# Performance work log

Measured on AMD Instinct MI355X. Metric: run time of the kernel, lower is better.

The kernel has to match this reference:

```python
import jax, jax.numpy as jnp
import numpy as np

BS, T, E, H, CU = 8, 1024, 512, 8, 6
HD = E // H
W_SCALE = 0.05  # keep pre-softmax logits in a sane range


def setup_inputs() -> dict:
    key = jax.random.key(0)
    ks = jax.random.split(key, 9)
    return {
        "x": jax.random.normal(ks[0], (BS, T, E), jnp.float32),
        "u": jax.random.normal(ks[1], (BS, CU, T, T), jnp.float32),
        "umask": jnp.zeros((BS, T, T, 1), jnp.bool_),
        "wq": jax.random.normal(ks[2], (E, E), jnp.float32) * W_SCALE,
        "wk": jax.random.normal(ks[3], (E, E), jnp.float32) * W_SCALE,
        "wv": jax.random.normal(ks[4], (E, E), jnp.float32) * W_SCALE,
        "wo": jax.random.normal(ks[5], (E, E), jnp.float32) * W_SCALE,
        "bo": jnp.zeros((E,), jnp.float32),
        "wu": jax.random.normal(ks[6], (H, CU), jnp.float32) * W_SCALE,
        "bu": jnp.zeros((H,), jnp.float32),
    }


def reference(x, u, umask, wq, wk, wv, wo, bo, wu, bu):
    bs, t, e = x.shape
    h, hd = H, HD
    scaling = hd ** (-0.5)

    # linear projections (torch Linear: y = x @ W^T), split heads -> [b, h, t, hd]
    def proj(w):
        return jnp.einsum('bte,fe->btf', x, w).reshape(bs, t, h, hd).transpose(0, 2, 1, 3)

    Q, K, V = proj(wq), proj(wk), proj(wv)

    # NOTE: faithful to source, which DIVIDES by head_dim**-0.5
    scores = jnp.einsum('bhqd,bhkd->bhqk', Q, K) / scaling

    # 1x1 conv bias projection: [b, cu, t, t] -> [b, h, t, t]
    ubias = jnp.einsum('bcij,hc->bhij', u, wu) + bu[None, :, None, None]
    # umask: [b, t, t, 1] -> swap dims 1 and 3 -> [b, 1, t, t]
    mask_t = jnp.transpose(umask, (0, 3, 2, 1))
    ubias = jnp.where(mask_t, -jnp.inf, ubias)
    scores = scores + ubias

    attn = jax.nn.softmax(scores, axis=-1)
    # dropout p=0.0 -> identity
    ctx = jnp.einsum('bhqk,bhkd->bqhd', attn, V).reshape(bs, t, e)
    out = jnp.einsum('bte,fe->btf', ctx, wo) + bo
    return (out, attn)
```

## Files before the change

### kernel.cpp

```cpp
#include <hip/hip_runtime.h>
#include <cmath>

#define BSZ 8
#define TT  1024
#define EE  512
#define HH  8
#define CUc 6
#define HDD 64

typedef __bf16 bf16;
typedef __attribute__((ext_vector_type(4))) float f32x4;
typedef __attribute__((ext_vector_type(8))) float f32x8;
typedef __attribute__((ext_vector_type(4))) bf16  bf16x4;
typedef __attribute__((ext_vector_type(8))) bf16  bf16x8;

static __device__ __forceinline__ f32x4 mfma16(bf16x8 a, bf16x8 b, f32x4 c) {
    return __builtin_amdgcn_mfma_f32_16x16x32_bf16(a, b, c, 0, 0, 0);
}
static __device__ __forceinline__ void glds16(const bf16* g, bf16* l) {
    __builtin_amdgcn_global_load_lds((const __attribute__((address_space(1))) void*)g,
                                     (__attribute__((address_space(3))) void*)l, 16, 0, 0);
}

__global__ __launch_bounds__(256) void k_split_all(
    const float* __restrict__ wq, const float* __restrict__ wk,
    const float* __restrict__ wv, const float* __restrict__ wo,
    bf16* __restrict__ wqh, bf16* __restrict__ wql,
    bf16* __restrict__ wkh, bf16* __restrict__ wkl,
    bf16* __restrict__ wvh, bf16* __restrict__ woh)
{
    const float* src; bf16* hi; bf16* lo;
    switch (blockIdx.y) {
        case 0: src = wq; hi = wqh; lo = wql;     break;
        case 1: src = wk; hi = wkh; lo = wkl;     break;
        case 2: src = wv; hi = wvh; lo = nullptr; break;
        default: src = wo; hi = woh; lo = nullptr; break;
    }
    const int i = (blockIdx.x * 256 + threadIdx.x) * 8;
    f32x8 v = *(const f32x8*)(src + i);
    bf16x8 h8, l8;
#pragma unroll
    for (int k = 0; k < 8; ++k) {
        bf16 h = (bf16)v[k];
        h8[k] = h;
        l8[k] = (bf16)(v[k] - (float)h);
    }
    *(bf16x8*)(hi + i) = h8;
    if (lo) *(bf16x8*)(lo + i) = l8;
}

__global__ __launch_bounds__(256) void k_proj2(
    const float* __restrict__ x,
    const bf16* __restrict__ wqh, const bf16* __restrict__ wql,
    const bf16* __restrict__ wkh, const bf16* __restrict__ wkl,
    const bf16* __restrict__ wvh,
    bf16* __restrict__ Qh, bf16* __restrict__ Ql,
    bf16* __restrict__ Kh, bf16* __restrict__ Kl,
    bf16* __restrict__ Vt)
{
    const int rb = blockIdx.x;
    const int cb = blockIdx.y;
    const int wid = threadIdx.x >> 6;
    const int l   = threadIdx.x & 63;
    const int lg = l >> 4, lr = l & 15;
    const int row = rb * 64 + wid * 16 + lr;

    f32x4 aq[4], ak[4], av[4];
#pragma unroll
    for (int c = 0; c < 4; ++c) {
        aq[c] = f32x4{0.f,0.f,0.f,0.f}; ak[c] = f32x4{0.f,0.f,0.f,0.f}; av[c] = f32x4{0.f,0.f,0.f,0.f};
    }

    for (int ks = 0; ks < 16; ++ks) {
        const int e0 = ks * 32 + lg * 8;
        f32x8 xv = *(const f32x8*)(x + (size_t)row * EE + e0);
        bf16x8 xh, xl;
#pragma unroll
        for (int i = 0; i < 8; ++i) {
            bf16 h = (bf16)xv[i];
            xh[i] = h;
            xl[i] = (bf16)(xv[i] - (float)h);
        }
#pragma unroll
        for (int c = 0; c < 4; ++c) {
            const int f = cb * 64 + c * 16 + lr;
            const size_t wo = (size_t)f * EE + e0;
            bf16x8 qh = *(const bf16x8*)(wqh + wo);
            bf16x8 ql = *(const bf16x8*)(wql + wo);
            bf16x8 kh = *(const bf16x8*)(wkh + wo);
            bf16x8 kl = *(const bf16x8*)(wkl + wo);
            bf16x8 vh = *(const bf16x8*)(wvh + wo);
            aq[c] = mfma16(xh, qh, aq[c]); aq[c] = mfma16(xh, ql, aq[c]); aq[c] = mfma16(xl, qh, aq[c]);
            ak[c] = mfma16(xh, kh, ak[c]); ak[c] = mfma16(xh, kl, ak[c]); ak[c] = mfma16(xl, kh, ak[c]);
            av[c] = mfma16(xh, vh, av[c]);
        }
    }

#pragma unroll
    for (int c = 0; c < 4; ++c)
#pragma unroll
        for (int r = 0; r < 4; ++r) {
            const int orow = rb * 64 + wid * 16 + lg * 4 + r;
            const int b = orow >> 10, t = orow & 1023;
            const int f = cb * 64 + c * 16 + lr;
            const int h = f >> 6, d = f & 63;
            const size_t idx = ((size_t)(b * HH + h) * TT + t) * HDD + d;
            float vq = aq[c][r];
            bf16 qhi = (bf16)vq; Qh[idx] = qhi; Ql[idx] = (bf16)(vq - (float)qhi);
            float vk = ak[c][r];
            bf16 khi = (bf16)vk; Kh[idx] = khi; Kl[idx] = (bf16)(vk - (float)khi);
            Vt[(((size_t)(b * HH + h) * HDD + d) * TT) + t] = (bf16)av[c][r];
        }
}

__global__ __launch_bounds__(256) void k_ubias2(
    const float* __restrict__ u, const unsigned char* __restrict__ umask,
    const float* __restrict__ wu, const float* __restrict__ bu,
    float* __restrict__ A)
{
    __shared__ __align__(16) unsigned char msk[64][64];
    const int b  = blockIdx.z;
    const int i0 = blockIdx.y * 64;
    const int j0 = blockIdx.x * 64;
    const int t  = threadIdx.x;

    {
        const int jj  = t >> 2;
        const int seg = (t & 3) * 16;
        *(uint4*)(&msk[jj][seg]) =
            *(const uint4*)(umask + ((size_t)b * TT + (j0 + jj)) * TT + i0 + seg);
    }
    float wuv[HH][CUc], buv[HH];
#pragma unroll
    for (int h = 0; h < HH; ++h) {
        buv[h] = bu[h];
#pragma unroll
        for (int c = 0; c < CUc; ++c) wuv[h][c] = wu[h * CUc + c];
    }
    __syncthreads();

    const int j = j0 + (t & 63);
    for (int ii = (t >> 6); ii < 64; ii += 4) {
        const int i = i0 + ii;
        float uv[CUc];
#pragma unroll
        for (int c = 0; c < CUc; ++c)
            uv[c] = u[(((size_t)b * CUc + c) * TT + i) * TT + j];
        const bool mk = msk[t & 63][ii] != 0;
#pragma unroll
        for (int h = 0; h < HH; ++h) {
            float v = buv[h];
#pragma unroll
            for (int c = 0; c < CUc; ++c) v += uv[c] * wuv[h][c];
            if (mk) v = -INFINITY;
            bf16* ub = (bf16*)(A + ((size_t)(b * HH + h) * TT + (i & ~15)) * TT);
            ub[(i & 15) * TT + j] = (bf16)v;
        }
    }
}

__global__ __launch_bounds__(512, 1) void kf10(
    const bf16* __restrict__ Qh, const bf16* __restrict__ Ql,
    const bf16* __restrict__ Kh, const bf16* __restrict__ Kl,
    const bf16* __restrict__ Vt,
    float* __restrict__ A, bf16* __restrict__ ctx)
{
    const int g  = blockIdx.x;
    const int b  = g & 7;
    const int hh = g >> 6;
    const int ib = (g >> 3) & 7;
    const int bh = b * HH + hh;
    const int i0 = ib * 128;
    const int w  = threadIdx.x >> 6;
    const int l  = threadIdx.x & 63;
    const int lg = l >> 4, lr = l & 15;
    const int i16c = ib * 8 + w;
    const int iw   = i0 + w * 16;

    __shared__ __align__(16) bf16 KHL[2][8192];
    __shared__ __align__(16) bf16 KLL[2][8192];
    __shared__ __align__(16) bf16 VL [2][8192];
    __shared__ __align__(16) bf16 P  [8][2048];
    __shared__ float mh[8][16][12];

    const bf16* KhG = Kh + (size_t)bh * TT * HDD;
    const bf16* KlG = Kl + (size_t)bh * TT * HDD;
    const bf16* VtG = Vt + (size_t)bh * HDD * TT;
    bf16* Aw = (bf16*)(A + ((size_t)bh * TT + i16c * 16) * TT);

    const bf16* qph = Qh + ((size_t)bh * TT + iw) * HDD;
    const bf16* qpl = Ql + ((size_t)bh * TT + iw) * HDD;
    bf16x8 qh0 = *(const bf16x8*)(qph + lr * HDD + lg * 8);
    bf16x8 qh1 = *(const bf16x8*)(qph + lr * HDD + 32 + lg * 8);
    bf16x8 ql0 = *(const bf16x8*)(qpl + lr * HDD + lg * 8);
    bf16x8 ql1 = *(const bf16x8*)(qpl + lr * HDD + 32 + lg * 8);

    auto stage = [&](int buf, int t) {
        const int j0 = t * 128;
#pragma unroll
        for (int k = 0; k < 6; ++k) {
            const int gu = w * 6 + k;
            if (gu < 16) {
                const int u = gu;
                const int jr = u * 8 + (l >> 3), s = l & 7;
                glds16(KhG + (size_t)(j0 + jr) * HDD + ((s ^ (jr & 7)) * 8),
                       &KHL[buf][u * 512]);
            } else if (gu < 32) {
                const int u = gu - 16;
                const int jr = u * 8 + (l >> 3), s = l & 7;
                glds16(KlG + (size_t)(j0 + jr) * HDD + ((s ^ (jr & 7)) * 8),
                       &KLL[buf][u * 512]);
            } else {
                const int u = gu - 32;
                const int d = u * 4 + (l >> 4), s = l & 15;
                const int q = (s & 8) | ((s ^ (d & 7)) & 7);
                glds16(VtG + (size_t)d * TT + j0 + q * 8,
                       &VL[buf][u * 512]);
            }
        }
    };

    float m_run[4], s_run[4];
    f32x4 cacc[4];
#pragma unroll
    for (int r = 0; r < 4; ++r) { m_run[r] = -INFINITY; s_run[r] = 0.f; }
#pragma unroll
    for (int dt = 0; dt < 4; ++dt) cacc[dt] = f32x4{0.f,0.f,0.f,0.f};

    stage(0, 0);
    __syncthreads();

    for (int t = 0; t < 8; ++t) {
        const int buf = t & 1;

        bf16x8 ubr[4];
#pragma unroll
        for (int q = 0; q < 4; ++q) {
            const int r = q * 4 + (l >> 4), s = l & 15;
            ubr[q] = *(const bf16x8*)(Aw + (size_t)r * TT + t * 128 + s * 8);
        }
        if (t < 7) stage(buf ^ 1, t + 1);

        f32x4 s8[8];
#pragma unroll
        for (int jt2 = 0; jt2 < 8; ++jt2) {
            const int jr = jt2 * 16 + lr;
            const int x7 = jr & 7;
            bf16x8 kh0 = *(const bf16x8*)&KHL[buf][jr * 64 + ((lg       ^ x7) * 8)];
            bf16x8 kh1 = *(const bf16x8*)&KHL[buf][jr * 64 + (((lg + 4) ^ x7) * 8)];
            bf16x8 kl0 = *(const bf16x8*)&KLL[buf][jr * 64 + ((lg       ^ x7) * 8)];
            bf16x8 kl1 = *(const bf16x8*)&KLL[buf][jr * 64 + (((lg + 4) ^ x7) * 8)];
            f32x4 acc = f32x4{0.f,0.f,0.f,0.f};
            acc = mfma16(qh0, kh0, acc); acc = mfma16(qh1, kh1, acc);
            acc = mfma16(qh0, kl0, acc); acc = mfma16(qh1, kl1, acc);
            acc = mfma16(ql0, kh0, acc); acc = mfma16(ql1, kh1, acc);
            s8[jt2] = acc;
        }

#pragma unroll
        for (int q = 0; q < 4; ++q) {
            const int r = q * 4 + (l >> 4), s = l & 15;
            const int slot = (s & 8) | ((s ^ (r & 7)) & 7);
            *(bf16x8*)&P[w][r * 128 + slot * 8] = ubr[q];
        }
#pragma unroll
        for (int jt2 = 0; jt2 < 8; ++jt2)
#pragma unroll
            for (int r = 0; r < 4; ++r) {
                const int row = lg * 4 + r, col = jt2 * 16 + lr;
                const int sg = col >> 3;
                const int slot = (sg & 8) | ((sg ^ (row & 7)) & 7);
                s8[jt2][r] = s8[jt2][r] * 8.0f + (float)P[w][row * 128 + slot * 8 + (col & 7)];
            }

        float tm[4];
#pragma unroll
        for (int r = 0; r < 4; ++r) {
            float mm = s8[0][r];
#pragma unroll
            for (int jt2 = 1; jt2 < 8; ++jt2) mm = fmaxf(mm, s8[jt2][r]);
            tm[r] = mm;
        }
#pragma unroll
        for (int off = 1; off < 16; off <<= 1)
#pragma unroll
            for (int r = 0; r < 4; ++r) tm[r] = fmaxf(tm[r], __shfl_xor(tm[r], off));
        float mnew[4], mexp[4], e[4];
#pragma unroll
        for (int r = 0; r < 4; ++r) {
            mnew[r] = fmaxf(m_run[r], tm[r]);
            mexp[r] = (mnew[r] == -INFINITY) ? 0.f : mnew[r];
            e[r]    = (m_run[r] == -INFINITY) ? 0.f : __expf(m_run[r] - mexp[r]);
            m_run[r] = mnew[r];
        }
#pragma unroll
        for (int dt = 0; dt < 4; ++dt)
#pragma unroll
            for (int r = 0; r < 4; ++r) cacc[dt][r] *= e[r];

        float psum[4] = {0.f, 0.f, 0.f, 0.f};
#pragma unroll
        for (int jt2 = 0; jt2 < 8; ++jt2)
#pragma unroll
            for (int r = 0; r < 4; ++r) {
                const float p = __expf(s8[jt2][r] - mexp[r]);
                psum[r] += p;
                const int row = lg * 4 + r, col = jt2 * 16 + lr;
                const int sg = col >> 3;
                const int slot = (sg & 8) | ((sg ^ (row & 7)) & 7);
                P[w][row * 128 + slot * 8 + (col & 7)] = (bf16)p;
            }
#pragma unroll
        for (int off = 1; off < 16; off <<= 1)
#pragma unroll
            for (int r = 0; r < 4; ++r) psum[r] += __shfl_xor(psum[r], off);
#pragma unroll
        for (int r = 0; r < 4; ++r) s_run[r] = s_run[r] * e[r] + psum[r];
        if (lr == 0)
#pragma unroll
            for (int r = 0; r < 4; ++r) mh[w][lg * 4 + r][t] = mnew[r];

#pragma unroll
        for (int q = 0; q < 4; ++q) {
            const int r = q * 4 + (l >> 4), s = l & 15;
            const int slot = (s & 8) | ((s ^ (r & 7)) & 7);
            bf16x8 pv = *(const bf16x8*)&P[w][r * 128 + slot * 8];
            *(bf16x8*)(Aw + (size_t)r * 2048 + 1024 + t * 128 + s * 8) = pv;
        }

#pragma unroll
        for (int ks = 0; ks < 4; ++ks) {
            const int sg = ks * 4 + lg;
            const int ps = (sg & 8) | ((sg ^ (lr & 7)) & 7);
            bf16x8 a = *(const bf16x8*)&P[w][lr * 128 + ps * 8];
#pragma unroll
            for (int dt = 0; dt < 4; ++dt) {
                const int d = dt * 16 + lr;
                const int vs = (sg & 8) | ((sg ^ (d & 7)) & 7);
                bf16x8 bv = *(const bf16x8*)&VL[buf][d * 128 + vs * 8];
                cacc[dt] = mfma16(a, bv, cacc[dt]);
            }
        }
        __syncthreads();
    }

    if (lr == 0)
#pragma unroll
        for (int r = 0; r < 4; ++r) mh[w][lg * 4 + r][8] = s_run[r];

    float invS[4], mfin[4];
#pragma unroll
    for (int q = 0; q < 4; ++q) {
        const int r = q * 4 + (l >> 4);
        mfin[q] = mh[w][r][7];
        invS[q] = 1.0f / mh[w][r][8];
    }
    float* Af = A + ((size_t)bh * TT + i16c * 16) * TT;
#pragma unroll
    for (int t = 0; t < 8; ++t) {
        bf16x8 pv[4];
        float fac[4];
#pragma unroll
        for (int q = 0; q < 4; ++q) {
            const int r = q * 4 + (l >> 4), s = l & 15;
            pv[q] = *(const bf16x8*)(Aw + (size_t)r * 2048 + 1024 + t * 128 + s * 8);
            fac[q] = __expf(mh[w][r][t] - mfin[q]) * invS[q];
        }
        asm volatile("s_waitcnt vmcnt(0)" ::: "memory");
#pragma unroll
        for (int q = 0; q < 4; ++q) {
            const int r = q * 4 + (l >> 4), s = l & 15;
            f32x4 o0, o1;
#pragma unroll
            for (int ee = 0; ee < 4; ++ee) {
                o0[ee] = (float)pv[q][ee]     * fac[q];
                o1[ee] = (float)pv[q][4 + ee] * fac[q];
            }
            *(f32x4*)(Af + (size_t)r * TT + t * 128 + s * 8)     = o0;
            *(f32x4*)(Af + (size_t)r * TT + t * 128 + s * 8 + 4) = o1;
        }
    }

#pragma unroll
    for (int r = 0; r < 4; ++r) {
        const float is = 1.0f / s_run[r];
        const int row = iw + lg * 4 + r;
#pragma unroll
        for (int dt = 0; dt < 4; ++dt)
            ctx[((size_t)b * TT + row) * EE + hh * HDD + dt * 16 + lr] = (bf16)(cacc[dt][r] * is);
    }
}

__global__ __launch_bounds__(256) void k_out2(
    const bf16* __restrict__ ctx, const bf16* __restrict__ woh,
    const float* __restrict__ bo, float* __restrict__ out)
{
    const int rb = blockIdx.x;
    const int cb = blockIdx.y;
    const int wid = threadIdx.x >> 6;
    const int l = threadIdx.x & 63;
    const int lg = l >> 4, lr = l & 15;
    const int row = rb * 64 + wid * 16 + lr;

    f32x4 acc[4];
#pragma unroll
    for (int c = 0; c < 4; ++c) acc[c] = f32x4{0.f,0.f,0.f,0.f};

    for (int ks = 0; ks < 16; ++ks) {
        const int e0 = ks * 32 + lg * 8;
        bf16x8 af = *(const bf16x8*)(ctx + (size_t)row * EE + e0);
#pragma unroll
        for (int c = 0; c < 4; ++c) {
            const int f = cb * 64 + c * 16 + lr;
            bf16x8 wf = *(const bf16x8*)(woh + (size_t)f * EE + e0);
            acc[c] = mfma16(af, wf, acc[c]);
        }
    }
#pragma unroll
    for (int c = 0; c < 4; ++c) {
        const int f = cb * 64 + c * 16 + lr;
        const float bov = bo[f];
#pragma unroll
        for (int r = 0; r < 4; ++r) {
            const int orow = rb * 64 + wid * 16 + lg * 4 + r;
            out[(size_t)orow * EE + f] = acc[c][r] + bov;
        }
    }
}

extern "C" void kernel_launch(void* const* d_in, const int* in_sizes, int n_in,
                              void* d_out, int out_size, void* d_ws, size_t ws_size,
                              hipStream_t stream)
{
    (void)in_sizes; (void)n_in; (void)out_size; (void)ws_size;
    const float* x  = (const float*)d_in[0];
    const float* u  = (const float*)d_in[1];
    const unsigned char* umask = (const unsigned char*)d_in[2];
    const float* wq = (const float*)d_in[3];
    const float* wk = (const float*)d_in[4];
    const float* wv = (const float*)d_in[5];
    const float* wo = (const float*)d_in[6];
    const float* bo = (const float*)d_in[7];
    const float* wu = (const float*)d_in[8];
    const float* bu = (const float*)d_in[9];

    float* out = (float*)d_out;
    float* A   = out + (size_t)BSZ * TT * EE;

    const size_t qs  = (size_t)BSZ * HH * TT * HDD;
    const size_t wsz = (size_t)EE * EE;
    bf16* Qh  = (bf16*)d_ws;
    bf16* Ql  = Qh + qs;
    bf16* Kh  = Ql + qs;
    bf16* Kl  = Kh + qs;
    bf16* Vt  = Kl + qs;
    bf16* ctx = Vt + qs;
    bf16* wqh = ctx + qs;
    bf16* wql = wqh + wsz;
    bf16* wkh = wql + wsz;
    bf16* wkl = wkh + wsz;
    bf16* wvh = wkl + wsz;
    bf16* woh = wvh + wsz;

    k_split_all<<<dim3(128, 4), 256, 0, stream>>>(wq, wk, wv, wo,
                                                  wqh, wql, wkh, wkl, wvh, woh);
    k_ubias2<<<dim3(16, 16, 8), 256, 0, stream>>>(u, umask, wu, bu, A);
    k_proj2 <<<dim3(128, 8), 256, 0, stream>>>(x, wqh, wql, wkh, wkl, wvh, Qh, Ql, Kh, Kl, Vt);
    kf10    <<<512, 512, 0, stream>>>(Qh, Ql, Kh, Kl, Vt, A, ctx);
    k_out2  <<<dim3(128, 8), 256, 0, stream>>>(ctx, woh, bo, out);
}
```

Baseline: 441.1 us.

## Halve attention key tile to 64 to cut LDS and allow more blocks per CU

The fused attention kernel now processes keys in 64-wide tiles over 16 iterations instead of 128-wide tiles over 8. This halves the shared-memory buffers for K, V and P, and the launch bound asks for 4 blocks per CU instead of 1, aiming at higher occupancy and better latency hiding. The cost is twice as many barriers and online-softmax rescale steps, plus a changed swizzle and a simpler final normalization pass. The projection and bias kernel launches are also swapped in order.

New measurement: 530.4 us. +20.2%, slower.

```diff
diff --git a/kernel.cpp b/kernel.cpp
--- a/kernel.cpp
+++ b/kernel.cpp
@@ -159,7 +159,7 @@
     }
 }
 
-__global__ __launch_bounds__(512, 1) void kf10(
+__global__ __launch_bounds__(512, 4) void kf10b(
     const bf16* __restrict__ Qh, const bf16* __restrict__ Ql,
     const bf16* __restrict__ Kh, const bf16* __restrict__ Kl,
     const bf16* __restrict__ Vt,
@@ -177,11 +177,11 @@
     const int i16c = ib * 8 + w;
     const int iw   = i0 + w * 16;
 
-    __shared__ __align__(16) bf16 KHL[2][8192];
-    __shared__ __align__(16) bf16 KLL[2][8192];
-    __shared__ __align__(16) bf16 VL [2][8192];
-    __shared__ __align__(16) bf16 P  [8][2048];
-    __shared__ float mh[8][16][12];
+    __shared__ __align__(16) bf16 KHL[2][4096];
+    __shared__ __align__(16) bf16 KLL[2][4096];
+    __shared__ __align__(16) bf16 VL [2][4096];
+    __shared__ __align__(16) bf16 P  [8][1024];
+    __shared__ float mh[8][16][18];
 
     const bf16* KhG = Kh + (size_t)bh * TT * HDD;
     const bf16* KlG = Kl + (size_t)bh * TT * HDD;
@@ -196,25 +196,23 @@
     bf16x8 ql1 = *(const bf16x8*)(qpl + lr * HDD + 32 + lg * 8);
 
     auto stage = [&](int buf, int t) {
-        const int j0 = t * 128;
-#pragma unroll
-        for (int k = 0; k < 6; ++k) {
-            const int gu = w * 6 + k;
-            if (gu < 16) {
-                const int u = gu;
-                const int jr = u * 8 + (l >> 3), s = l & 7;
+        const int j0 = t * 64;
+#pragma unroll
+        for (int k = 0; k < 3; ++k) {
+            const int gu = w * 3 + k;
+            if (gu < 8) {
+                const int jr = gu * 8 + (l >> 3), s = l & 7;
                 glds16(KhG + (size_t)(j0 + jr) * HDD + ((s ^ (jr & 7)) * 8),
-                       &KHL[buf][u * 512]);
-            } else if (gu < 32) {
-                const int u = gu - 16;
+                       &KHL[buf][gu * 512]);
+            } else if (gu < 16) {
+                const int u = gu - 8;
                 const int jr = u * 8 + (l >> 3), s = l & 7;
                 glds16(KlG + (size_t)(j0 + jr) * HDD + ((s ^ (jr & 7)) * 8),
                        &KLL[buf][u * 512]);
             } else {
-                const int u = gu - 32;
-                const int d = u * 4 + (l >> 4), s = l & 15;
-                const int q = (s & 8) | ((s ^ (d & 7)) & 7);
-                glds16(VtG + (size_t)d * TT + j0 + q * 8,
+                const int u = gu - 16;
+                const int d = u * 8 + (l >> 3), s = l & 7;
+                glds16(VtG + (size_t)d * TT + j0 + ((s ^ (d & 7)) * 8),
                        &VL[buf][u * 512]);
             }
         }
@@ -230,20 +228,20 @@
     stage(0, 0);
     __syncthreads();
 
-    for (int t = 0; t < 8; ++t) {
+    for (int t = 0; t < 16; ++t) {
         const int buf = t & 1;
 
-        bf16x8 ubr[4];
-#pragma unroll
-        for (int q = 0; q < 4; ++q) {
-            const int r = q * 4 + (l >> 4), s = l & 15;
-            ubr[q] = *(const bf16x8*)(Aw + (size_t)r * TT + t * 128 + s * 8);
-        }
-        if (t < 7) stage(buf ^ 1, t + 1);
-
-        f32x4 s8[8];
-#pragma unroll
-        for (int jt2 = 0; jt2 < 8; ++jt2) {
+        bf16x8 ubr[2];
+#pragma unroll
+        for (int q = 0; q < 2; ++q) {
+            const int r = q * 8 + (l >> 3), s = l & 7;
+            ubr[q] = *(const bf16x8*)(Aw + (size_t)r * TT + t * 64 + s * 8);
+        }
+        if (t < 15) stage(buf ^ 1, t + 1);
+
+        f32x4 s8[4];
+#pragma unroll
+        for (int jt2 = 0; jt2 < 4; ++jt2) {
             const int jr = jt2 * 16 + lr;
             const int x7 = jr & 7;
             bf16x8 kh0 = *(const bf16x8*)&KHL[buf][jr * 64 + ((lg       ^ x7) * 8)];
@@ -258,19 +256,18 @@
         }
 
 #pragma unroll
-        for (int q = 0; q < 4; ++q) {
-            const int r = q * 4 + (l >> 4), s = l & 15;
-            const int slot = (s & 8) | ((s ^ (r & 7)) & 7);
-            *(bf16x8*)&P[w][r * 128 + slot * 8] = ubr[q];
-        }
-#pragma unroll
-        for (int jt2 = 0; jt2 < 8; ++jt2)
+        for (int q = 0; q < 2; ++q) {
+            const int r = q * 8 + (l >> 3), s = l & 7;
+            *(bf16x8*)&P[w][r * 64 + ((s ^ (r & 7)) * 8)] = ubr[q];
+        }
+#pragma unroll
+        for (int jt2 = 0; jt2 < 4; ++jt2)
 #pragma unroll
             for (int r = 0; r < 4; ++r) {
                 const int row = lg * 4 + r, col = jt2 * 16 + lr;
                 const int sg = col >> 3;
-                const int slot = (sg & 8) | ((sg ^ (row & 7)) & 7);
-                s8[jt2][r] = s8[jt2][r] * 8.0f + (float)P[w][row * 128 + slot * 8 + (col & 7)];
+                s8[jt2][r] = s8[jt2][r] * 8.0f +
+                    (float)P[w][row * 64 + ((sg ^ (row & 7)) * 8) + (col & 7)];
             }
 
         float tm[4];
@@ -278,7 +275,7 @@
         for (int r = 0; r < 4; ++r) {
             float mm = s8[0][r];
 #pragma unroll
-            for (int jt2 = 1; jt2 < 8; ++jt2) mm = fmaxf(mm, s8[jt2][r]);
+            for (int jt2 = 1; jt2 < 4; ++jt2) mm = fmaxf(mm, s8[jt2][r]);
             tm[r] = mm;
         }
 #pragma unroll
@@ -300,15 +297,14 @@
 
         float psum[4] = {0.f, 0.f, 0.f, 0.f};
 #pragma unroll
-        for (int jt2 = 0; jt2 < 8; ++jt2)
+        for (int jt2 = 0; jt2 < 4; ++jt2)
 #pragma unroll
             for (int r = 0; r < 4; ++r) {
                 const float p = __expf(s8[jt2][r] - mexp[r]);
                 psum[r] += p;
                 const int row = lg * 4 + r, col = jt2 * 16 + lr;
                 const int sg = col >> 3;
-                const int slot = (sg & 8) | ((sg ^ (row & 7)) & 7);
-                P[w][row * 128 + slot * 8 + (col & 7)] = (bf16)p;
+                P[w][row * 64 + ((sg ^ (row & 7)) * 8) + (col & 7)] = (bf16)p;
             }
 #pragma unroll
         for (int off = 1; off < 16; off <<= 1)
@@ -321,23 +317,20 @@
             for (int r = 0; r < 4; ++r) mh[w][lg * 4 + r][t] = mnew[r];
 
 #pragma unroll
-        for (int q = 0; q < 4; ++q) {
-            const int r = q * 4 + (l >> 4), s = l & 15;
-            const int slot = (s & 8) | ((s ^ (r & 7)) & 7);
-            bf16x8 pv = *(const bf16x8*)&P[w][r * 128 + slot * 8];
-            *(bf16x8*)(Aw + (size_t)r * 2048 + 1024 + t * 128 + s * 8) = pv;
-        }
-
-#pragma unroll
-        for (int ks = 0; ks < 4; ++ks) {
+        for (int q = 0; q < 2; ++q) {
+            const int r = q * 8 + (l >> 3), s = l & 7;
+            bf16x8 pv = *(const bf16x8*)&P[w][r * 64 + ((s ^ (r & 7)) * 8)];
+            *(bf16x8*)(Aw + (size_t)r * 2048 + 1024 + t * 64 + s * 8) = pv;
+        }
+
+#pragma unroll
+        for (int ks = 0; ks < 2; ++ks) {
             const int sg = ks * 4 + lg;
-            const int ps = (sg & 8) | ((sg ^ (lr & 7)) & 7);
-            bf16x8 a = *(const bf16x8*)&P[w][lr * 128 + ps * 8];
+            bf16x8 a = *(const bf16x8*)&P[w][lr * 64 + ((sg ^ (lr & 7)) * 8)];
 #pragma unroll
             for (int dt = 0; dt < 4; ++dt) {
                 const int d = dt * 16 + lr;
-                const int vs = (sg & 8) | ((sg ^ (d & 7)) & 7);
-                bf16x8 bv = *(const bf16x8*)&VL[buf][d * 128 + vs * 8];
+                bf16x8 bv = *(const bf16x8*)&VL[buf][d * 64 + ((sg ^ (d & 7)) * 8)];
                 cacc[dt] = mfma16(a, bv, cacc[dt]);
             }
         }
@@ -346,38 +339,24 @@
 
     if (lr == 0)
 #pragma unroll
-        for (int r = 0; r < 4; ++r) mh[w][lg * 4 + r][8] = s_run[r];
-
-    float invS[4], mfin[4];
-#pragma unroll
-    for (int q = 0; q < 4; ++q) {
-        const int r = q * 4 + (l >> 4);
-        mfin[q] = mh[w][r][7];
-        invS[q] = 1.0f / mh[w][r][8];
-    }
+        for (int r = 0; r < 4; ++r) mh[w][lg * 4 + r][16] = s_run[r];
+
     float* Af = A + ((size_t)bh * TT + i16c * 16) * TT;
 #pragma unroll
-    for (int t = 0; t < 8; ++t) {
-        bf16x8 pv[4];
-        float fac[4];
-#pragma unroll
-        for (int q = 0; q < 4; ++q) {
-            const int r = q * 4 + (l >> 4), s = l & 15;
-            pv[q] = *(const bf16x8*)(Aw + (size_t)r * 2048 + 1024 + t * 128 + s * 8);
-            fac[q] = __expf(mh[w][r][t] - mfin[q]) * invS[q];
-        }
-        asm volatile("s_waitcnt vmcnt(0)" ::: "memory");
-#pragma unroll
-        for (int q = 0; q < 4; ++q) {
-            const int r = q * 4 + (l >> 4), s = l & 15;
+    for (int t = 0; t < 16; ++t) {
+#pragma unroll
+        for (int q = 0; q < 2; ++q) {
+            const int r = q * 8 + (l >> 3), s = l & 7;
+            bf16x8 pv = *(const bf16x8*)(Aw + (size_t)r * 2048 + 1024 + t * 64 + s * 8);
+            const float fac = __expf(mh[w][r][t] - mh[w][r][15]) / mh[w][r][16];
             f32x4 o0, o1;
 #pragma unroll
             for (int ee = 0; ee < 4; ++ee) {
-                o0[ee] = (float)pv[q][ee]     * fac[q];
-                o1[ee] = (float)pv[q][4 + ee] * fac[q];
+                o0[ee] = (float)pv[ee]     * fac;
+                o1[ee] = (float)pv[4 + ee] * fac;
             }
-            *(f32x4*)(Af + (size_t)r * TT + t * 128 + s * 8)     = o0;
-            *(f32x4*)(Af + (size_t)r * TT + t * 128 + s * 8 + 4) = o1;
+            *(f32x4*)(Af + (size_t)r * TT + t * 64 + s * 8)     = o0;
+            *(f32x4*)(Af + (size_t)r * TT + t * 64 + s * 8 + 4) = o1;
         }
     }
 
@@ -464,8 +443,8 @@
 
     k_split_all<<<dim3(128, 4), 256, 0, stream>>>(wq, wk, wv, wo,
                                                   wqh, wql, wkh, wkl, wvh, woh);
+    k_proj2 <<<dim3(128, 8), 256, 0, stream>>>(x, wqh, wql, wkh, wkl, wvh, Qh, Ql, Kh, Kl, Vt);
     k_ubias2<<<dim3(16, 16, 8), 256, 0, stream>>>(u, umask, wu, bu, A);
-    k_proj2 <<<dim3(128, 8), 256, 0, stream>>>(x, wqh, wql, wkh, wkl, wvh, Qh, Ql, Kh, Kl, Vt);
-    kf10    <<<512, 512, 0, stream>>>(Qh, Ql, Kh, Kl, Vt, A, ctx);
+    kf10b   <<<512, 512, 0, stream>>>(Qh, Ql, Kh, Kl, Vt, A, ctx);
     k_out2  <<<dim3(128, 8), 256, 0, stream>>>(ctx, woh, bo, out);
 }
```

## Single-buffer K/V tiles and halve P scratch to fit multiple blocks per CU

Applied to the files above, without the earlier changes.

The flash-attention kernel drops double-buffered K/V LDS staging and shrinks the per-wave P scratch to half width. The P@V product and the attention write-back are now split into two 64-column halves. Launch bounds change from 1 to 4 blocks per CU, and s_setprio is raised around the MFMA sections. The aim is higher occupancy so that other resident blocks hide memory latency. The cost is that the load-to-compute overlap inside a block is lost, because staging is now bracketed by two barriers per tile.

Result: slower. 635.0 us (+44.0%).

```diff
diff --git a/kernel.cpp b/kernel.cpp
--- a/kernel.cpp
+++ b/kernel.cpp
@@ -159,7 +159,7 @@
     }
 }
 
-__global__ __launch_bounds__(512, 1) void kf10(
+__global__ __launch_bounds__(512, 4) void kf10c(
     const bf16* __restrict__ Qh, const bf16* __restrict__ Ql,
     const bf16* __restrict__ Kh, const bf16* __restrict__ Kl,
     const bf16* __restrict__ Vt,
@@ -177,11 +177,11 @@
     const int i16c = ib * 8 + w;
     const int iw   = i0 + w * 16;
 
-    __shared__ __align__(16) bf16 KHL[2][8192];
-    __shared__ __align__(16) bf16 KLL[2][8192];
-    __shared__ __align__(16) bf16 VL [2][8192];
-    __shared__ __align__(16) bf16 P  [8][2048];
-    __shared__ float mh[8][16][12];
+    __shared__ __align__(16) bf16 KHL[8192];
+    __shared__ __align__(16) bf16 KLL[8192];
+    __shared__ __align__(16) bf16 VL [8192];
+    __shared__ __align__(16) bf16 P  [8][1024];
+    __shared__ float mh[8][16][10];
 
     const bf16* KhG = Kh + (size_t)bh * TT * HDD;
     const bf16* KlG = Kl + (size_t)bh * TT * HDD;
@@ -195,27 +195,23 @@
     bf16x8 ql0 = *(const bf16x8*)(qpl + lr * HDD + lg * 8);
     bf16x8 ql1 = *(const bf16x8*)(qpl + lr * HDD + 32 + lg * 8);
 
-    auto stage = [&](int buf, int t) {
+    auto stage = [&](int t) {
         const int j0 = t * 128;
 #pragma unroll
         for (int k = 0; k < 6; ++k) {
             const int gu = w * 6 + k;
             if (gu < 16) {
-                const int u = gu;
-                const int jr = u * 8 + (l >> 3), s = l & 7;
-                glds16(KhG + (size_t)(j0 + jr) * HDD + ((s ^ (jr & 7)) * 8),
-                       &KHL[buf][u * 512]);
+                const int jr = gu * 8 + (l >> 3), s = l & 7;
+                glds16(KhG + (size_t)(j0 + jr) * HDD + ((s ^ (jr & 7)) * 8), &KHL[gu * 512]);
             } else if (gu < 32) {
                 const int u = gu - 16;
                 const int jr = u * 8 + (l >> 3), s = l & 7;
-                glds16(KlG + (size_t)(j0 + jr) * HDD + ((s ^ (jr & 7)) * 8),
-                       &KLL[buf][u * 512]);
+                glds16(KlG + (size_t)(j0 + jr) * HDD + ((s ^ (jr & 7)) * 8), &KLL[u * 512]);
             } else {
                 const int u = gu - 32;
                 const int d = u * 4 + (l >> 4), s = l & 15;
                 const int q = (s & 8) | ((s ^ (d & 7)) & 7);
-                glds16(VtG + (size_t)d * TT + j0 + q * 8,
-                       &VL[buf][u * 512]);
+                glds16(VtG + (size_t)d * TT + j0 + q * 8, &VL[u * 512]);
             }
         }
     };
@@ -227,51 +223,75 @@
 #pragma unroll
     for (int dt = 0; dt < 4; ++dt) cacc[dt] = f32x4{0.f,0.f,0.f,0.f};
 
-    stage(0, 0);
-    __syncthreads();
-
     for (int t = 0; t < 8; ++t) {
-        const int buf = t & 1;
-
         bf16x8 ubr[4];
 #pragma unroll
         for (int q = 0; q < 4; ++q) {
             const int r = q * 4 + (l >> 4), s = l & 15;
             ubr[q] = *(const bf16x8*)(Aw + (size_t)r * TT + t * 128 + s * 8);
         }
-        if (t < 7) stage(buf ^ 1, t + 1);
+        __syncthreads();
+        stage(t);
+        __syncthreads();
+
+        bf16 ubsc[8][4];
+        {
+            const int s = l & 15;
+            if (s < 8) {
+#pragma unroll
+                for (int q = 0; q < 4; ++q) {
+                    const int r = q * 4 + (l >> 4);
+                    *(bf16x8*)&P[w][r * 64 + ((s ^ (r & 7)) * 8)] = ubr[q];
+                }
+            }
+#pragma unroll
+            for (int jt2 = 0; jt2 < 4; ++jt2)
+#pragma unroll
+                for (int r = 0; r < 4; ++r) {
+                    const int row = lg * 4 + r, col = jt2 * 16 + lr;
+                    const int sgc = col >> 3;
+                    ubsc[jt2][r] = P[w][row * 64 + ((sgc ^ (row & 7)) * 8) + (col & 7)];
+                }
+            if (s >= 8) {
+#pragma unroll
+                for (int q = 0; q < 4; ++q) {
+                    const int r = q * 4 + (l >> 4);
+                    *(bf16x8*)&P[w][r * 64 + (((s - 8) ^ (r & 7)) * 8)] = ubr[q];
+                }
+            }
+#pragma unroll
+            for (int jt2 = 4; jt2 < 8; ++jt2)
+#pragma unroll
+                for (int r = 0; r < 4; ++r) {
+                    const int row = lg * 4 + r, cl = jt2 * 16 + lr - 64;
+                    const int sgc = cl >> 3;
+                    ubsc[jt2][r] = P[w][row * 64 + ((sgc ^ (row & 7)) * 8) + (cl & 7)];
+                }
+        }
 
         f32x4 s8[8];
+        __builtin_amdgcn_s_setprio(1);
 #pragma unroll
         for (int jt2 = 0; jt2 < 8; ++jt2) {
             const int jr = jt2 * 16 + lr;
             const int x7 = jr & 7;
-            bf16x8 kh0 = *(const bf16x8*)&KHL[buf][jr * 64 + ((lg       ^ x7) * 8)];
-            bf16x8 kh1 = *(const bf16x8*)&KHL[buf][jr * 64 + (((lg + 4) ^ x7) * 8)];
-            bf16x8 kl0 = *(const bf16x8*)&KLL[buf][jr * 64 + ((lg       ^ x7) * 8)];
-            bf16x8 kl1 = *(const bf16x8*)&KLL[buf][jr * 64 + (((lg + 4) ^ x7) * 8)];
+            bf16x8 kh0 = *(const bf16x8*)&KHL[jr * 64 + ((lg       ^ x7) * 8)];
+            bf16x8 kh1 = *(const bf16x8*)&KHL[jr * 64 + (((lg + 4) ^ x7) * 8)];
+            bf16x8 kl0 = *(const bf16x8*)&KLL[jr * 64 + ((lg       ^ x7) * 8)];
+            bf16x8 kl1 = *(const bf16x8*)&KLL[jr * 64 + (((lg + 4) ^ x7) * 8)];
             f32x4 acc = f32x4{0.f,0.f,0.f,0.f};
             acc = mfma16(qh0, kh0, acc); acc = mfma16(qh1, kh1, acc);
             acc = mfma16(qh0, kl0, acc); acc = mfma16(qh1, kl1, acc);
             acc = mfma16(ql0, kh0, acc); acc = mfma16(ql1, kh1, acc);
             s8[jt2] = acc;
         }
-
-#pragma unroll
-        for (int q = 0; q < 4; ++q) {
-            const int r = q * 4 + (l >> 4), s = l & 15;
-            const int slot = (s & 8) | ((s ^ (r & 7)) & 7);
-            *(bf16x8*)&P[w][r * 128 + slot * 8] = ubr[q];
-        }
+        __builtin_amdgcn_s_setprio(0);
+
 #pragma unroll
         for (int jt2 = 0; jt2 < 8; ++jt2)
 #pragma unroll
-            for (int r = 0; r < 4; ++r) {
-                const int row = lg * 4 + r, col = jt2 * 16 + lr;
-                const int sg = col >> 3;
-                const int slot = (sg & 8) | ((sg ^ (row & 7)) & 7);
-                s8[jt2][r] = s8[jt2][r] * 8.0f + (float)P[w][row * 128 + slot * 8 + (col & 7)];
-            }
+            for (int r = 0; r < 4; ++r)
+                s8[jt2][r] = s8[jt2][r] * 8.0f + (float)ubsc[jt2][r];
 
         float tm[4];
 #pragma unroll
@@ -305,10 +325,7 @@
             for (int r = 0; r < 4; ++r) {
                 const float p = __expf(s8[jt2][r] - mexp[r]);
                 psum[r] += p;
-                const int row = lg * 4 + r, col = jt2 * 16 + lr;
-                const int sg = col >> 3;
-                const int slot = (sg & 8) | ((sg ^ (row & 7)) & 7);
-                P[w][row * 128 + slot * 8 + (col & 7)] = (bf16)p;
+                s8[jt2][r] = p;
             }
 #pragma unroll
         for (int off = 1; off < 16; off <<= 1)
@@ -321,32 +338,72 @@
             for (int r = 0; r < 4; ++r) mh[w][lg * 4 + r][t] = mnew[r];
 
 #pragma unroll
-        for (int q = 0; q < 4; ++q) {
-            const int r = q * 4 + (l >> 4), s = l & 15;
-            const int slot = (s & 8) | ((s ^ (r & 7)) & 7);
-            bf16x8 pv = *(const bf16x8*)&P[w][r * 128 + slot * 8];
-            *(bf16x8*)(Aw + (size_t)r * 2048 + 1024 + t * 128 + s * 8) = pv;
-        }
-
-#pragma unroll
-        for (int ks = 0; ks < 4; ++ks) {
+        for (int jt2 = 0; jt2 < 4; ++jt2)
+#pragma unroll
+            for (int r = 0; r < 4; ++r) {
+                const int row = lg * 4 + r, col = jt2 * 16 + lr;
+                const int sgc = col >> 3;
+                P[w][row * 64 + ((sgc ^ (row & 7)) * 8) + (col & 7)] = (bf16)s8[jt2][r];
+            }
+        __builtin_amdgcn_s_setprio(1);
+#pragma unroll
+        for (int ks = 0; ks < 2; ++ks) {
             const int sg = ks * 4 + lg;
-            const int ps = (sg & 8) | ((sg ^ (lr & 7)) & 7);
-            bf16x8 a = *(const bf16x8*)&P[w][lr * 128 + ps * 8];
+            bf16x8 a = *(const bf16x8*)&P[w][lr * 64 + ((sg ^ (lr & 7)) * 8)];
 #pragma unroll
             for (int dt = 0; dt < 4; ++dt) {
                 const int d = dt * 16 + lr;
                 const int vs = (sg & 8) | ((sg ^ (d & 7)) & 7);
-                bf16x8 bv = *(const bf16x8*)&VL[buf][d * 128 + vs * 8];
+                bf16x8 bv = *(const bf16x8*)&VL[d * 128 + vs * 8];
                 cacc[dt] = mfma16(a, bv, cacc[dt]);
             }
         }
-        __syncthreads();
+        __builtin_amdgcn_s_setprio(0);
+        {
+            const int pr = l >> 2, sg = (l & 3) * 2;
+            bf16x8 p0 = *(const bf16x8*)&P[w][pr * 64 + ((sg       ^ (pr & 7)) * 8)];
+            bf16x8 p1 = *(const bf16x8*)&P[w][pr * 64 + (((sg + 1) ^ (pr & 7)) * 8)];
+            *(bf16x8*)(Aw + (size_t)pr * 2048 + 1024 + t * 128 + sg * 8)     = p0;
+            *(bf16x8*)(Aw + (size_t)pr * 2048 + 1024 + t * 128 + sg * 8 + 8) = p1;
+        }
+
+#pragma unroll
+        for (int jt2 = 4; jt2 < 8; ++jt2)
+#pragma unroll
+            for (int r = 0; r < 4; ++r) {
+                const int row = lg * 4 + r, cl = jt2 * 16 + lr - 64;
+                const int sgc = cl >> 3;
+                P[w][row * 64 + ((sgc ^ (row & 7)) * 8) + (cl & 7)] = (bf16)s8[jt2][r];
+            }
+        __builtin_amdgcn_s_setprio(1);
+#pragma unroll
+        for (int ks = 2; ks < 4; ++ks) {
+            const int sgl = (ks - 2) * 4 + lg;
+            const int sgv = ks * 4 + lg;
+            bf16x8 a = *(const bf16x8*)&P[w][lr * 64 + ((sgl ^ (lr & 7)) * 8)];
+#pragma unroll
+            for (int dt = 0; dt < 4; ++dt) {
+                const int d = dt * 16 + lr;
+                const int vs = (sgv & 8) | ((sgv ^ (d & 7)) & 7);
+                bf16x8 bv = *(const bf16x8*)&VL[d * 128 + vs * 8];
+                cacc[dt] = mfma16(a, bv, cacc[dt]);
+            }
+        }
+        __builtin_amdgcn_s_setprio(0);
+        {
+            const int pr = l >> 2, sg = (l & 3) * 2;
+            bf16x8 p0 = *(const bf16x8*)&P[w][pr * 64 + ((sg       ^ (pr & 7)) * 8)];
+            bf16x8 p1 = *(const bf16x8*)&P[w][pr * 64 + (((sg + 1) ^ (pr & 7)) * 8)];
+            *(bf16x8*)(Aw + (size_t)pr * 2048 + 1024 + t * 128 + 64 + sg * 8)     = p0;
+            *(bf16x8*)(Aw + (size_t)pr * 2048 + 1024 + t * 128 + 64 + sg * 8 + 8) = p1;
+        }
     }
 
     if (lr == 0)
 #pragma unroll
         for (int r = 0; r < 4; ++r) mh[w][lg * 4 + r][8] = s_run[r];
+    __syncthreads();
+    asm volatile("s_waitcnt vmcnt(0)" ::: "memory");
 
     float invS[4], mfin[4];
 #pragma unroll
@@ -366,7 +423,6 @@
             pv[q] = *(const bf16x8*)(Aw + (size_t)r * 2048 + 1024 + t * 128 + s * 8);
             fac[q] = __expf(mh[w][r][t] - mfin[q]) * invS[q];
         }
-        asm volatile("s_waitcnt vmcnt(0)" ::: "memory");
 #pragma unroll
         for (int q = 0; q < 4; ++q) {
             const int r = q * 4 + (l >> 4), s = l & 15;
@@ -466,6 +522,6 @@
                                                   wqh, wql, wkh, wkl, wvh, woh);
     k_ubias2<<<dim3(16, 16, 8), 256, 0, stream>>>(u, umask, wu, bu, A);
     k_proj2 <<<dim3(128, 8), 256, 0, stream>>>(x, wqh, wql, wkh, wkl, wvh, Qh, Ql, Kh, Kl, Vt);
-    kf10    <<<512, 512, 0, stream>>>(Qh, Ql, Kh, Kl, Vt, A, ctx);
+    kf10c   <<<512, 512, 0, stream>>>(Qh, Ql, Kh, Kl, Vt, A, ctx);
     k_out2  <<<dim3(128, 8), 256, 0, stream>>>(ctx, woh, bo, out);
 }
```
